# Kernel optimization log

Hardware: AMD Instinct MI355X
Metric: run time of the kernel (lower is better)

## Reference

```python
import jax, jax.numpy as jnp
import numpy as np

B, S, D = 16, 2048, 768  # batch, padded subword length, roberta hidden dim


def setup_inputs() -> dict:
    key = jax.random.key(0)
    k1, k2 = jax.random.split(key)
    robert_embed = jax.random.normal(k1, (B, S, D), dtype=jnp.float32)
    # Non-decreasing per-row segment ids: contiguous runs of equal ids are the
    # subword spans that merge_list would average; singleton runs pass through.
    seg_ids = jnp.sort(jax.random.randint(k2, (B, S), 0, S, dtype=jnp.int32), axis=-1)
    return {"robert_embed": robert_embed, "seg_ids": seg_ids}


def reference(robert_embed, seg_ids):
    # Segment-mean gather/scatter: out[b, w] = mean_{p: seg_ids[b,p]==w} x[b, p]
    b, s, d = robert_embed.shape
    w = s  # output word slots (<= s); empty slots yield zeros
    flat_seg = (seg_ids + (w * jnp.arange(b, dtype=seg_ids.dtype))[:, None]).reshape(-1)
    x_flat = robert_embed.reshape(-1, d)
    sums = jax.ops.segment_sum(x_flat, flat_seg, num_segments=b * w)  # [b*w, d]
    counts = jax.ops.segment_sum(
        jnp.ones((b * s,), dtype=robert_embed.dtype), flat_seg, num_segments=b * w
    )
    out = sums / jnp.maximum(counts, 1)[:, None]
    return out.reshape(b, w, d)
```

## Files before the change

kernel.cpp:

```cpp
#include <hip/hip_runtime.h>

#define BB 16
#define SS 2048
#define DD 768
#define D4 (DD / 4)

__global__ __launch_bounds__(256) void seg_mean_fused(
    const float* __restrict__ x,
    const int*   __restrict__ seg,
    float*       __restrict__ out) {
    int lane = threadIdx.x & 63;
    int wave = threadIdx.x >> 6;
    int bw   = (blockIdx.x << 2) + wave;
    int b    = bw >> 11;
    int w    = bw & (SS - 1);
    const int* srow = seg + (b << 11);

    int v1 = srow[lane << 5];
    int k  = __popcll(__ballot(v1 < w));
    int base2 = (k == 0) ? 0 : ((k - 1) << 5);

    int idx2 = base2 + lane;
    int v2 = 0x7fffffff;
    if (lane < 33 && idx2 < SS) v2 = srow[idx2];
    int k2 = __popcll(__ballot(v2 < w));
    int lo = base2 + k2;
    unsigned long long meq = __ballot(v2 == w);
    int cwin  = (int)__builtin_ctzll(~(meq >> k2));
    int avail = 33 - k2;

    int c;
    if (cwin < avail) {
        c = cwin;
    } else {
        c = avail;
        int p = base2 + 33;
        for (;;) {
            int idx = p + lane;
            int v   = (idx < SS) ? srow[idx] : -1;
            unsigned long long m  = __ballot(v == w);
            unsigned long long nm = ~m;
            if (nm) { c += (int)__builtin_ctzll(nm); break; }
            c += 64; p += 64;
        }
    }

    float4* outp = (float4*)(out + (size_t)bw * DD);
    if (c == 0) {
        float4 z = make_float4(0.f, 0.f, 0.f, 0.f);
        outp[lane]       = z;
        outp[lane + 64]  = z;
        outp[lane + 128] = z;
        return;
    }

    const float4* xp = (const float4*)(x + ((size_t)b * SS + (size_t)lo) * DD);
    float4 a0 = xp[lane];
    float4 a1 = xp[lane + 64];
    float4 a2 = xp[lane + 128];
    if (c > 1) {
        const float4* xr = xp + D4;
        float4 r0 = xr[lane], r1 = xr[lane + 64], r2 = xr[lane + 128];
        for (int j = 2; j < c; ++j) {
            const float4* xn = xp + (size_t)j * D4;
            float4 t0 = xn[lane], t1 = xn[lane + 64], t2 = xn[lane + 128];
            a0.x += r0.x; a0.y += r0.y; a0.z += r0.z; a0.w += r0.w;
            a1.x += r1.x; a1.y += r1.y; a1.z += r1.z; a1.w += r1.w;
            a2.x += r2.x; a2.y += r2.y; a2.z += r2.z; a2.w += r2.w;
            r0 = t0; r1 = t1; r2 = t2;
        }
        a0.x += r0.x; a0.y += r0.y; a0.z += r0.z; a0.w += r0.w;
        a1.x += r1.x; a1.y += r1.y; a1.z += r1.z; a1.w += r1.w;
        a2.x += r2.x; a2.y += r2.y; a2.z += r2.z; a2.w += r2.w;
    }
    float inv = 1.0f / (float)c;
    a0.x *= inv; a0.y *= inv; a0.z *= inv; a0.w *= inv;
    a1.x *= inv; a1.y *= inv; a1.z *= inv; a1.w *= inv;
    a2.x *= inv; a2.y *= inv; a2.z *= inv; a2.w *= inv;
    outp[lane]       = a0;
    outp[lane + 64]  = a1;
    outp[lane + 128] = a2;
}

extern "C" void kernel_launch(void* const* d_in, const int* in_sizes, int n_in,
                              void* d_out, int out_size, void* d_ws, size_t ws_size,
                              hipStream_t stream) {
    const float* x   = (const float*)d_in[0];
    const int*   seg = (const int*)d_in[1];
    float* out = (float*)d_out;

    int nBlocks = (BB * SS) / 4;
    seg_mean_fused<<<nBlocks, 256, 0, stream>>>(x, seg, out);
}
```

Measured before the change: 179.2 us.

## Iterate over input segment starts per wave instead of searching per output slot

Parallelisation moves from one wave per output slot, which binary-searches the segment ids, to one wave per chunk of 8 input positions. Each wave detects segment starts in its chunk, averages each run it owns, and writes zeros for the empty output slots up to the next segment id. This drops the per-output search over seg ids and the redundant ballots for empty slots. In exchange the work per wave becomes imbalanced, since gaps of zero rows are written serially by the wave that owns the previous segment, and the grid is 8x smaller.

```diff
diff --git a/kernel.cpp b/kernel.cpp
--- a/kernel.cpp
+++ b/kernel.cpp
@@ -4,82 +4,95 @@
 #define SS 2048
 #define DD 768
 #define D4 (DD / 4)
+#define CH 8
 
-__global__ __launch_bounds__(256) void seg_mean_fused(
+__global__ __launch_bounds__(256) void seg_mean_stream(
     const float* __restrict__ x,
     const int*   __restrict__ seg,
     float*       __restrict__ out) {
     int lane = threadIdx.x & 63;
     int wave = threadIdx.x >> 6;
-    int bw   = (blockIdx.x << 2) + wave;
-    int b    = bw >> 11;
-    int w    = bw & (SS - 1);
-    const int* srow = seg + (b << 11);
+    int gw   = (blockIdx.x << 2) + wave;
+    int p0   = gw * CH;
+    int b    = p0 >> 11;
+    int q0   = p0 & (SS - 1);
+    const int*   srow = seg + (b << 11);
+    const float* xb   = x   + (size_t)(b << 11) * DD;
+    float*       ob   = out + (size_t)(b << 11) * DD;
 
-    int v1 = srow[lane << 5];
-    int k  = __popcll(__ballot(v1 < w));
-    int base2 = (k == 0) ? 0 : ((k - 1) << 5);
+    bool startl = false;
+    if (lane < CH) {
+        int p   = q0 + lane;
+        int myv = srow[p];
+        int pv  = (p == 0) ? (myv ^ 1) : srow[p - 1];
+        startl  = (myv != pv);
+    }
+    unsigned long long smask = __ballot(startl);
 
-    int idx2 = base2 + lane;
-    int v2 = 0x7fffffff;
-    if (lane < 33 && idx2 < SS) v2 = srow[idx2];
-    int k2 = __popcll(__ballot(v2 < w));
-    int lo = base2 + k2;
-    unsigned long long meq = __ballot(v2 == w);
-    int cwin  = (int)__builtin_ctzll(~(meq >> k2));
-    int avail = 33 - k2;
+    const float4 zz = make_float4(0.f, 0.f, 0.f, 0.f);
 
-    int c;
-    if (cwin < avail) {
-        c = cwin;
-    } else {
-        c = avail;
-        int p = base2 + 33;
-        for (;;) {
-            int idx = p + lane;
-            int v   = (idx < SS) ? srow[idx] : -1;
-            unsigned long long m  = __ballot(v == w);
-            unsigned long long nm = ~m;
-            if (nm) { c += (int)__builtin_ctzll(nm); break; }
-            c += 64; p += 64;
+    if (q0 == 0) {
+        int first = srow[0];
+        for (int z = 0; z < first; ++z) {
+            float4* zp = (float4*)(ob + (size_t)z * DD);
+            zp[lane] = zz; zp[lane + 64] = zz; zp[lane + 128] = zz;
         }
     }
 
-    float4* outp = (float4*)(out + (size_t)bw * DD);
-    if (c == 0) {
-        float4 z = make_float4(0.f, 0.f, 0.f, 0.f);
-        outp[lane]       = z;
-        outp[lane + 64]  = z;
-        outp[lane + 128] = z;
-        return;
-    }
+    while (smask) {
+        int i = (int)__builtin_ctzll(smask);
+        smask &= smask - 1;
+        int s = q0 + i;
+        int v = srow[s];
+        int e;
+        if (smask) {
+            e = q0 + (int)__builtin_ctzll(smask);
+        } else {
+            e = q0 + CH;
+            for (;;) {
+                int idx = e + lane;
+                int vv  = (idx < SS) ? srow[idx] : (v ^ 1);
+                unsigned long long m  = __ballot(vv == v);
+                unsigned long long nm = ~m;
+                if (nm) { e += (int)__builtin_ctzll(nm); break; }
+                e += 64;
+            }
+        }
+        int c     = e - s;
+        int vnext = (e < SS) ? srow[e] : SS;
 
-    const float4* xp = (const float4*)(x + ((size_t)b * SS + (size_t)lo) * DD);
-    float4 a0 = xp[lane];
-    float4 a1 = xp[lane + 64];
-    float4 a2 = xp[lane + 128];
-    if (c > 1) {
-        const float4* xr = xp + D4;
-        float4 r0 = xr[lane], r1 = xr[lane + 64], r2 = xr[lane + 128];
-        for (int j = 2; j < c; ++j) {
-            const float4* xn = xp + (size_t)j * D4;
-            float4 t0 = xn[lane], t1 = xn[lane + 64], t2 = xn[lane + 128];
+        const float4* xp = (const float4*)(xb + (size_t)s * DD);
+        float4 a0 = xp[lane];
+        float4 a1 = xp[lane + 64];
+        float4 a2 = xp[lane + 128];
+        if (c > 1) {
+            const float4* xr = xp + D4;
+            float4 r0 = xr[lane], r1 = xr[lane + 64], r2 = xr[lane + 128];
+            for (int j = 2; j < c; ++j) {
+                const float4* xn = xp + (size_t)j * D4;
+                float4 t0 = xn[lane], t1 = xn[lane + 64], t2 = xn[lane + 128];
+                a0.x += r0.x; a0.y += r0.y; a0.z += r0.z; a0.w += r0.w;
+                a1.x += r1.x; a1.y += r1.y; a1.z += r1.z; a1.w += r1.w;
+                a2.x += r2.x; a2.y += r2.y; a2.z += r2.z; a2.w += r2.w;
+                r0 = t0; r1 = t1; r2 = t2;
+            }
             a0.x += r0.x; a0.y += r0.y; a0.z += r0.z; a0.w += r0.w;
             a1.x += r1.x; a1.y += r1.y; a1.z += r1.z; a1.w += r1.w;
             a2.x += r2.x; a2.y += r2.y; a2.z += r2.z; a2.w += r2.w;
-            r0 = t0; r1 = t1; r2 = t2;
         }
-        a0.x += r0.x; a0.y += r0.y; a0.z += r0.z; a0.w += r0.w;
-        a1.x += r1.x; a1.y += r1.y; a1.z += r1.z; a1.w += r1.w;
-        a2.x += r2.x; a2.y += r2.y; a2.z += r2.z; a2.w += r2.w;
+        float inv = 1.0f / (float)c;
+        a0.x *= inv; a0.y *= inv; a0.z *= inv; a0.w *= inv;
+        a1.x *= inv; a1.y *= inv; a1.z *= inv; a1.w *= inv;
+        a2.x *= inv; a2.y *= inv; a2.z *= inv; a2.w *= inv;
+
+        float4* op = (float4*)(ob + (size_t)v * DD);
+        op[lane] = a0; op[lane + 64] = a1; op[lane + 128] = a2;
+
+        for (int z = v + 1; z < vnext; ++z) {
+            float4* zp = (float4*)(ob + (size_t)z * DD);
+            zp[lane] = zz; zp[lane + 64] = zz; zp[lane + 128] = zz;
+        }
     }
-    float inv = 1.0f / (float)c;
-    a0.x *= inv; a0.y *= inv; a0.z *= inv; a0.w *= inv;
-    a1.x *= inv; a1.y *= inv; a1.z *= inv; a1.w *= inv;
-    a2.x *= inv; a2.y *= inv; a2.z *= inv; a2.w *= inv;
-    outp[lane]       = a0;
-    outp[lane + 64]  = a1;
-    outp[lane + 128] = a2;
 }
 
 extern "C" void kernel_launch(void* const* d_in, const int* in_sizes, int n_in,
@@ -89,6 +102,6 @@
     const int*   seg = (const int*)d_in[1];
     float* out = (float*)d_out;
 
-    int nBlocks = (BB * SS) / 4;
-    seg_mean_fused<<<nBlocks, 256, 0, stream>>>(x, seg, out);
+    int nBlocks = (BB * SS) / (4 * CH);
+    seg_mean_stream<<<nBlocks, 256, 0, stream>>>(x, seg, out);
 }
```

Result: slower. 185.4 us (+3.5%).
